# Performance work log

Measured on AMD Instinct MI355X. Metric: run time of the kernel, lower is better.

Reference implementation:

```python
import jax, jax.numpy as jnp
import numpy as np

B, S, D = 4, 2048, 1024
MULT = 4
INNER = MULT * D
E = 4          # n_expert
K = 1          # top-k
ALPHA = 0.5


def setup_inputs() -> dict:
    key = jax.random.key(0)
    ks = jax.random.split(key, 8)
    std = 0.02
    x = jax.random.normal(ks[0], (B, S, D), jnp.float32)
    W1 = jax.random.normal(ks[1], (D, INNER), jnp.float32) * std
    b1 = jnp.zeros((INNER,), jnp.float32)
    W2 = jax.random.normal(ks[2], (INNER, D), jnp.float32) * std
    b2 = jnp.zeros((D,), jnp.float32)
    Wg = jax.random.normal(ks[3], (D, E), jnp.float32) * std
    ew1 = jax.random.normal(ks[4], (E, D, INNER), jnp.float32) * std
    ew3 = jax.random.normal(ks[5], (E, D, INNER), jnp.float32) * std
    ew2 = jax.random.normal(ks[6], (E, INNER, D), jnp.float32) * std
    return {"x": x, "W1": W1, "b1": b1, "W2": W2, "b2": b2,
            "Wg": Wg, "ew1": ew1, "ew3": ew3, "ew2": ew2}


def reference(x, W1, b1, W2, b2, Wg, ew1, ew3, ew2):
    # Dense branch: Linear -> GELU (exact, torch default) -> Linear
    y_dense = jax.nn.gelu(x @ W1 + b1, approximate=False) @ W2 + b2

    # MoE branch: top-k softmax routing, SwiGLU experts
    logits = x @ Wg                                   # [B,S,E]
    probs = jax.nn.softmax(logits, axis=-1)
    topv, topi = jax.lax.top_k(probs, K)              # [B,S,K]
    gates = topv / jnp.sum(topv, axis=-1, keepdims=True)  # renormalize top-k
    onehot = jax.nn.one_hot(topi, E, dtype=x.dtype)   # [B,S,K,E]
    combine = jnp.sum(gates[..., None] * onehot, axis=-2)  # [B,S,E]

    y_moe = jnp.zeros_like(x)
    for e in range(E):  # small fixed expert count
        h = jax.nn.silu(x @ ew1[e]) * (x @ ew3[e])    # [B,S,INNER]
        y_moe = y_moe + combine[..., e:e + 1] * (h @ ew2[e])

    # Load-balancing aux loss: E * sum_e f_e * P_e
    frac = jnp.mean(jnp.sum(onehot, axis=-2), axis=(0, 1)) / K  # [E]
    pmean = jnp.mean(probs, axis=(0, 1))                        # [E]
    aux = E * jnp.sum(frac * pmean)

    y = ALPHA * y_dense + (1.0 - ALPHA) * y_moe
    return (y, aux)
```

## Files before the change

### kernel.cpp

```cpp
#include <hip/hip_runtime.h>
#include <hip/hip_bf16.h>


static constexpr int MT = 8192;
static constexpr int DD = 1024;
static constexpr int DI = 4096;

typedef float f32x4 __attribute__((ext_vector_type(4)));
typedef __bf16 bf16x8 __attribute__((ext_vector_type(8)));
typedef unsigned short u16;

__device__ __forceinline__ u16 f2bf(float f) {
    union { __hip_bfloat16 b; u16 u; } v;
    v.b = __float2bfloat16(f);
    return v.u;
}

__device__ __forceinline__ void gload_lds16(const void* g, void* l) {
    __builtin_amdgcn_global_load_lds(
        (const __attribute__((address_space(1))) void*)g,
        (__attribute__((address_space(3))) void*)l, 16, 0, 0);
}

__device__ __forceinline__ float gelu_f(float v) {
    return 0.5f * v * (1.0f + erff(v * 0.70710678118654752f));
}
__device__ __forceinline__ float silu_f(float v) {
    return v / (1.0f + expf(-v));
}

#define FENCE() asm volatile("" ::: "memory")
#define BARRIER() do { FENCE(); __builtin_amdgcn_s_barrier(); FENCE(); } while (0)
#define WAIT_LGKM0() asm volatile("s_waitcnt lgkmcnt(0)" ::: "memory")

__global__ void __launch_bounds__(256) transpose_cvt(
    const float* __restrict__ src, u16* __restrict__ dst, int K, int N,
    int pack, int packOff, size_t srcMatStride, size_t dstMatStride) {
    __shared__ u16 t[64][72];
    const float* s = src + (size_t)blockIdx.z * srcMatStride;
    u16* d = dst + (size_t)blockIdx.z * dstMatStride;
    int n0 = blockIdx.x * 64, k0 = blockIdx.y * 64;
    int tid = threadIdx.x;
    int c = tid & 15;
    int r = tid >> 4;
#pragma unroll
    for (int p = 0; p < 4; ++p) {
        int k = r + p * 16;
        float4 v = *(const float4*)(s + (size_t)(k0 + k) * N + n0 + c * 4);
        t[c * 4 + 0][k] = f2bf(v.x);
        t[c * 4 + 1][k] = f2bf(v.y);
        t[c * 4 + 2][k] = f2bf(v.z);
        t[c * 4 + 3][k] = f2bf(v.w);
    }
    __syncthreads();
    int n = tid >> 2, kc = (tid & 3) * 16;
    const uint4* p0 = (const uint4*)&t[n][kc];
    uint4 a = p0[0], b = p0[1];
    int gn = n0 + n;
    int dr = pack ? ((gn >> 5) * 64 + (gn & 31) + packOff) : gn;
    uint4* o = (uint4*)(d + (size_t)dr * K + k0 + kc);
    o[0] = a; o[1] = b;
}

__global__ void __launch_bounds__(256) gate_kernel(
    const float* __restrict__ x, const float* __restrict__ Wg,
    float* __restrict__ psum_blk, int* __restrict__ expertA) {
    int w = threadIdx.x >> 6, l = threadIdx.x & 63;
    int t = blockIdx.x * 4 + w;
    const float* xr = x + (size_t)t * DD;
    double a0 = 0, a1 = 0, a2 = 0, a3 = 0;
#pragma unroll
    for (int i = 0; i < 4; ++i) {
        int k = i * 256 + l * 4;
        float4 xv = *(const float4*)(xr + k);
        float4 w0 = *(const float4*)(Wg + (size_t)(k + 0) * 4);
        float4 w1 = *(const float4*)(Wg + (size_t)(k + 1) * 4);
        float4 w2 = *(const float4*)(Wg + (size_t)(k + 2) * 4);
        float4 w3 = *(const float4*)(Wg + (size_t)(k + 3) * 4);
        a0 += (double)xv.x * w0.x + (double)xv.y * w1.x + (double)xv.z * w2.x + (double)xv.w * w3.x;
        a1 += (double)xv.x * w0.y + (double)xv.y * w1.y + (double)xv.z * w2.y + (double)xv.w * w3.y;
        a2 += (double)xv.x * w0.z + (double)xv.y * w1.z + (double)xv.z * w2.z + (double)xv.w * w3.z;
        a3 += (double)xv.x * w0.w + (double)xv.y * w1.w + (double)xv.z * w2.w + (double)xv.w * w3.w;
    }
#pragma unroll
    for (int o = 32; o; o >>= 1) {
        a0 += __shfl_down(a0, o); a1 += __shfl_down(a1, o);
        a2 += __shfl_down(a2, o); a3 += __shfl_down(a3, o);
    }
    __shared__ float wps[4][4];
    if (l == 0) {
        double lg[4] = {a0, a1, a2, a3};
        int best = 0;
#pragma unroll
        for (int e = 1; e < 4; ++e) if (lg[e] > lg[best]) best = e;
        double m = lg[best], s = 0, p[4];
#pragma unroll
        for (int e = 0; e < 4; ++e) { p[e] = exp(lg[e] - m); s += p[e]; }
#pragma unroll
        for (int e = 0; e < 4; ++e) wps[w][e] = (float)(p[e] / s);
        expertA[t] = best;
    }
    __syncthreads();
    if (threadIdx.x < 4)
        psum_blk[blockIdx.x * 4 + threadIdx.x] =
            wps[0][threadIdx.x] + wps[1][threadIdx.x] + wps[2][threadIdx.x] + wps[3][threadIdx.x];
}

__global__ void __launch_bounds__(1024) build_lists(
    const int* __restrict__ expertA, const float* __restrict__ psum_blk,
    int* __restrict__ dstArr, int* __restrict__ rev,
    int* __restrict__ offsets, float* __restrict__ auxOut) {
    __shared__ int sc[4][1024];
    __shared__ float fs[1024];
    __shared__ float psum_s[4];
    __shared__ int tot_s[4], off_s[4];
    int tid = threadIdx.x;
    int le[8]; int c[4] = {0, 0, 0, 0};
#pragma unroll
    for (int i = 0; i < 8; ++i) { int e = expertA[tid * 8 + i]; le[i] = e; c[e]++; }
#pragma unroll
    for (int e = 0; e < 4; ++e) sc[e][tid] = c[e];
    __syncthreads();
    for (int o = 1; o < 1024; o <<= 1) {
        int v[4];
#pragma unroll
        for (int e = 0; e < 4; ++e) v[e] = (tid >= o) ? sc[e][tid - o] : 0;
        __syncthreads();
#pragma unroll
        for (int e = 0; e < 4; ++e) if (tid >= o) sc[e][tid] += v[e];
        __syncthreads();
    }
    if (tid == 0) {
        int o = 0;
#pragma unroll
        for (int e = 0; e < 4; ++e) {
            tot_s[e] = sc[e][1023]; off_s[e] = o; offsets[e] = o; o += tot_s[e];
        }
        offsets[4] = o;
    }
    __syncthreads();
    int base[4];
#pragma unroll
    for (int e = 0; e < 4; ++e) base[e] = off_s[e] + sc[e][tid] - c[e];
#pragma unroll
    for (int i = 0; i < 8; ++i) {
        int e = le[i]; int d = base[e]++; int t = tid * 8 + i;
        dstArr[t] = d; rev[d] = t;
    }
    float ps[4];
#pragma unroll
    for (int e = 0; e < 4; ++e)
        ps[e] = psum_blk[(2 * tid) * 4 + e] + psum_blk[(2 * tid + 1) * 4 + e];
    for (int e = 0; e < 4; ++e) {
        fs[tid] = ps[e]; __syncthreads();
        for (int o = 512; o; o >>= 1) { if (tid < o) fs[tid] += fs[tid + o]; __syncthreads(); }
        if (tid == 0) psum_s[e] = fs[0];
        __syncthreads();
    }
    if (tid == 0) {
        float a = 0;
#pragma unroll
        for (int e = 0; e < 4; ++e)
            a += ((float)tot_s[e] * (1.f / 8192.f)) * (psum_s[e] * (1.f / 8192.f));
        auxOut[0] = 4.f * a;
    }
}

__global__ void __launch_bounds__(256) gather_kernel(
    const float* __restrict__ x, const int* __restrict__ dstArr,
    u16* __restrict__ xb, u16* __restrict__ xg) {
    int w = threadIdx.x >> 6, l = threadIdx.x & 63;
    int t = blockIdx.x * 4 + w;
    int dst = dstArr[t];
    const float* xr = x + (size_t)t * DD;
#pragma unroll
    for (int i = 0; i < 4; ++i) {
        int k = i * 256 + l * 4;
        float4 v = *(const float4*)(xr + k);
        ushort4 u;
        u.x = f2bf(v.x); u.y = f2bf(v.y); u.z = f2bf(v.z); u.w = f2bf(v.w);
        *(ushort4*)(xb + (size_t)t * DD + k) = u;
        *(ushort4*)(xg + (size_t)dst * DD + k) = u;
    }
}

template <int MODE, int NF>
__global__ void __launch_bounds__(512, 2) gemm8(
    const u16* __restrict__ A, const u16* __restrict__ Bw,
    const float* __restrict__ bias,
    u16* __restrict__ outB, float* __restrict__ outF,
    const int* __restrict__ offsets, const int* __restrict__ rev,
    int N, int K) {
    constexpr int BN   = NF * 64;
    constexpr int WCW  = NF * 16;
    constexpr int AELT = 2 * 256 * 32;
    constexpr int BUFE = AELT + 2 * BN * 32;
    constexpr int NIB  = NF / 2;
    __shared__ u16 lds[2 * BUFE];

    const int tid = threadIdx.x;
    const int w = tid >> 6, l = tid & 63;
    const int lr = l & 15, lg = l >> 4;
    const int wr = w >> 2, wc = w & 3;

    int rowBase, rowsValid = 256;
    const u16* Bp = Bw;
    if constexpr (MODE >= 2) {
        int e = blockIdx.z;
        int off = offsets[e], cnt = offsets[e + 1] - off;
        if ((int)blockIdx.y * 256 >= cnt) return;
        rowBase = off + blockIdx.y * 256;
        rowsValid = cnt - (int)blockIdx.y * 256;
        if (rowsValid > 256) rowsValid = 256;
        Bp = Bw + (size_t)e * ((size_t)(MODE == 2 ? 2 : 1) * DD * DI);
    } else {
        rowBase = blockIdx.y * 256;
    }
    const int colBase = blockIdx.x * BN;
    const int NT = K >> 6;

    auto stageA = [&](int kt, int b, int ks) {
        const int kk = (kt << 6) + (ks << 5);
#pragma unroll
        for (int i = 0; i < 2; ++i) {
            int o = ((w << 1) + i) * 512 + (l << 3);
            int o2 = o ^ (((o >> 8) & 1) << 4);
            gload_lds16(A + (size_t)(rowBase + (o2 >> 5)) * K + kk + (o2 & 31),
                        &lds[b * BUFE + ks * 8192 + ((w << 1) + i) * 512]);
        }
    };
    auto stageB = [&](int kt, int b, int ks) {
        const int kk = (kt << 6) + (ks << 5);
#pragma unroll
        for (int i = 0; i < NIB; ++i) {
            int o = (w * NIB + i) * 512 + (l << 3);
            int o2 = o ^ (((o >> 8) & 1) << 4);
            gload_lds16(Bp + (size_t)(colBase + (o2 >> 5)) * K + kk + (o2 & 31),
                        &lds[b * BUFE + AELT + ks * (BN * 32) + (w * NIB + i) * 512]);
        }
    };

#define WAIT_VMB() do { \
    if constexpr (NF == 4) asm volatile("s_waitcnt vmcnt(4)" ::: "memory"); \
    else                   asm volatile("s_waitcnt vmcnt(3)" ::: "memory"); \
} while (0)

#define READBF(b_, ks_) do { \
    _Pragma("unroll") \
    for (int n = 0; n < NF; ++n) { \
        int e_ = (wc * WCW + n * 16 + lr) * 32 + lg * 8; \
        e_ ^= ((e_ >> 8) & 1) << 4; \
        bf[n] = *(const bf16x8*)&lds[(b_) * BUFE + AELT + (ks_) * (BN * 32) + e_]; \
    } \
} while (0)

#define READAF(b_, ks_, mq_) do { \
    _Pragma("unroll") \
    for (int m = 0; m < 4; ++m) { \
        int e_ = (wr * 128 + ((mq_) * 4 + m) * 16 + lr) * 32 + lg * 8; \
        e_ ^= ((e_ >> 8) & 1) << 4; \
        af[m] = *(const bf16x8*)&lds[(b_) * BUFE + (ks_) * 8192 + e_]; \
    } \
} while (0)

#define DOMFMA(mq_) do { \
    __builtin_amdgcn_s_setprio(1); \
    _Pragma("unroll") \
    for (int m = 0; m < 4; ++m) \
    _Pragma("unroll") \
    for (int n = 0; n < NF; ++n) \
        acc[(mq_) * 4 + m][n] = __builtin_amdgcn_mfma_f32_16x16x32_bf16( \
            bf[n], af[m], acc[(mq_) * 4 + m][n], 0, 0, 0); \
    __builtin_amdgcn_s_setprio(0); \
} while (0)

    f32x4 acc[8][NF];
#pragma unroll
    for (int m = 0; m < 8; ++m)
#pragma unroll
        for (int n = 0; n < NF; ++n) acc[m][n] = (f32x4){0.f, 0.f, 0.f, 0.f};
    bf16x8 af[4], bf[NF];

    stageA(0, 0, 0); stageB(0, 0, 0); stageA(0, 0, 1); stageB(0, 0, 1);
    stageA(1, 1, 0); stageB(1, 1, 0);
    WAIT_VMB();
    BARRIER();

    for (int t = 0; t < NT; ++t) {
        const int cb = t & 1, nb = cb ^ 1;
        const int tp1 = (t + 1 < NT) ? t + 1 : NT - 1;
        const int tp2 = (t + 2 < NT) ? t + 2 : NT - 1;
        READBF(cb, 0); READAF(cb, 0, 0); stageA(tp1, nb, 1);
        BARRIER(); WAIT_LGKM0(); DOMFMA(0); BARRIER();
        READAF(cb, 0, 1); stageB(tp1, nb, 1);
        BARRIER(); WAIT_LGKM0(); DOMFMA(1); BARRIER();
        READBF(cb, 1); READAF(cb, 1, 0); stageA(tp2, cb, 0);
        BARRIER(); WAIT_LGKM0(); DOMFMA(0); BARRIER();
        READAF(cb, 1, 1); stageB(tp2, cb, 0);
        BARRIER(); WAIT_LGKM0(); DOMFMA(1);
        WAIT_VMB();
        BARRIER();
    }

#pragma unroll
    for (int m = 0; m < 8; ++m) {
        int rloc = wr * 128 + m * 16 + lr;
        if (MODE >= 2 && rloc >= rowsValid) continue;
        size_t grow = (size_t)(rowBase + rloc);
        if constexpr (MODE == 2) {
#pragma unroll
            for (int n = 0; n < 2; ++n) {
                int col = (colBase >> 1) + wc * 32 + n * 16 + lg * 4;
                f32x4 v1 = acc[m][n], v3 = acc[m][n + 2];
                ushort4 u;
                u.x = f2bf(silu_f(v1[0]) * v3[0]);
                u.y = f2bf(silu_f(v1[1]) * v3[1]);
                u.z = f2bf(silu_f(v1[2]) * v3[2]);
                u.w = f2bf(silu_f(v1[3]) * v3[3]);
                *(ushort4*)(outB + grow * N + col) = u;
            }
        } else {
#pragma unroll
            for (int n = 0; n < NF; ++n) {
                int col = colBase + wc * WCW + n * 16 + lg * 4;
                f32x4 v = acc[m][n];
                if constexpr (MODE == 0) {
                    f32x4 bb = *(const f32x4*)(bias + col);
                    ushort4 u;
                    u.x = f2bf(gelu_f(v[0] + bb[0]));
                    u.y = f2bf(gelu_f(v[1] + bb[1]));
                    u.z = f2bf(gelu_f(v[2] + bb[2]));
                    u.w = f2bf(gelu_f(v[3] + bb[3]));
                    *(ushort4*)(outB + grow * N + col) = u;
                } else if constexpr (MODE == 1) {
                    f32x4 bb = *(const f32x4*)(bias + col);
                    f32x4 r;
#pragma unroll
                    for (int j = 0; j < 4; ++j) r[j] = 0.5f * (v[j] + bb[j]);
                    *(f32x4*)(outF + grow * N + col) = r;
                } else {
                    int tok = rev[grow];
                    f32x4* p = (f32x4*)(outF + (size_t)tok * N + col);
                    f32x4 o = *p;
#pragma unroll
                    for (int j = 0; j < 4; ++j) o[j] += 0.5f * v[j];
                    *p = o;
                }
            }
        }
    }
#undef WAIT_VMB
#undef READBF
#undef READAF
#undef DOMFMA
}

extern "C" void kernel_launch(void* const* d_in, const int* in_sizes, int n_in,
                              void* d_out, int out_size, void* d_ws, size_t ws_size,
                              hipStream_t stream) {
    const float* x   = (const float*)d_in[0];
    const float* W1  = (const float*)d_in[1];
    const float* b1  = (const float*)d_in[2];
    const float* W2  = (const float*)d_in[3];
    const float* b2  = (const float*)d_in[4];
    const float* Wg  = (const float*)d_in[5];
    const float* ew1 = (const float*)d_in[6];
    const float* ew3 = (const float*)d_in[7];
    const float* ew2 = (const float*)d_in[8];
    float* y = (float*)d_out;
    float* auxOut = y + (size_t)MT * DD;

    char* ws = (char*)d_ws;
    size_t off = 0;
    auto take = [&](size_t b) -> void* {
        void* p = ws + off;
        off += (b + 255) & ~(size_t)255;
        return p;
    };
    u16* W1t   = (u16*)take((size_t)DI * DD * 2);
    u16* W2t   = (u16*)take((size_t)DI * DD * 2);
    u16* ew13t = (u16*)take((size_t)4 * 2 * DI * DD * 2);
    u16* ew2t  = (u16*)take((size_t)4 * DI * DD * 2);
    u16* xb    = (u16*)take((size_t)MT * DD * 2);
    u16* xg    = (u16*)take((size_t)(MT + 256) * DD * 2);
    u16* hd    = (u16*)take((size_t)(MT + 256) * DI * 2);
    int* expertA  = (int*)take(MT * 4);
    int* dstArr   = (int*)take(MT * 4);
    int* revA     = (int*)take(MT * 4);
    float* psum_blk = (float*)take(2048 * 4 * 4);
    int* offsets  = (int*)take(64);
    u16* hg = hd;

    if (ws_size < off) return;

    dim3 blk(256);
    transpose_cvt<<<dim3(64, 16, 1), blk, 0, stream>>>(W1,  W1t,  DD, DI, 0, 0,  (size_t)DD * DI, (size_t)DD * DI);
    transpose_cvt<<<dim3(64, 16, 4), blk, 0, stream>>>(ew1, ew13t, DD, DI, 1, 0,  (size_t)DD * DI, (size_t)2 * DD * DI);
    transpose_cvt<<<dim3(64, 16, 4), blk, 0, stream>>>(ew3, ew13t, DD, DI, 1, 32, (size_t)DD * DI, (size_t)2 * DD * DI);
    transpose_cvt<<<dim3(16, 64, 1), blk, 0, stream>>>(W2,  W2t,  DI, DD, 0, 0,  (size_t)DD * DI, (size_t)DD * DI);
    transpose_cvt<<<dim3(16, 64, 4), blk, 0, stream>>>(ew2, ew2t, DI, DD, 0, 0,  (size_t)DD * DI, (size_t)DD * DI);
    gate_kernel<<<2048, 256, 0, stream>>>(x, Wg, psum_blk, expertA);
    build_lists<<<1, 1024, 0, stream>>>(expertA, psum_blk, dstArr, revA, offsets, auxOut);
    gather_kernel<<<2048, 256, 0, stream>>>(x, dstArr, xb, xg);
    gemm8<0, 4><<<dim3(DI / 256, MT / 256), dim3(512), 0, stream>>>(
        xb, W1t, b1, hd, nullptr, nullptr, nullptr, DI, DD);
    gemm8<1, 2><<<dim3(DD / 128, MT / 256), dim3(512), 0, stream>>>(
        hd, W2t, b2, nullptr, y, nullptr, nullptr, DD, DI);
    gemm8<2, 4><<<dim3(2 * DI / 256, MT / 256, 4), dim3(512), 0, stream>>>(
        xg, ew13t, nullptr, hg, nullptr, offsets, nullptr, DI, DD);
    gemm8<3, 2><<<dim3(DD / 128, MT / 256, 4), dim3(512), 0, stream>>>(
        hg, ew2t, nullptr, nullptr, y, offsets, revA, DD, DI);
}
```

Before: 641.1 us.

## Reuse gathered activations for dense path and use simpler down-projection GEMM

The dense first GEMM now reads the expert-sorted bf16 copy xg instead of a separate row-ordered xb, so the gather kernel writes only one bf16 copy of x. The dense hidden rows therefore come out in sorted order, and the new dense down-projection scatters them back through the reverse index. Both down-projection GEMMs (K=4096, N=1024) move from the 256x128, 512-thread double-buffered gemm8 to a new single-buffered 128x128, 256-thread kernel, which gives more blocks on the narrow output. The cost is no overlap between global loads and MFMA in the new kernel, plus scattered row writes in the dense output.

```diff
diff --git a/kernel.cpp b/kernel.cpp
--- a/kernel.cpp
+++ b/kernel.cpp
@@ -168,7 +168,7 @@
 
 __global__ void __launch_bounds__(256) gather_kernel(
     const float* __restrict__ x, const int* __restrict__ dstArr,
-    u16* __restrict__ xb, u16* __restrict__ xg) {
+    u16* __restrict__ xg) {
     int w = threadIdx.x >> 6, l = threadIdx.x & 63;
     int t = blockIdx.x * 4 + w;
     int dst = dstArr[t];
@@ -179,7 +179,6 @@
         float4 v = *(const float4*)(xr + k);
         ushort4 u;
         u.x = f2bf(v.x); u.y = f2bf(v.y); u.z = f2bf(v.z); u.w = f2bf(v.w);
-        *(ushort4*)(xb + (size_t)t * DD + k) = u;
         *(ushort4*)(xg + (size_t)dst * DD + k) = u;
     }
 }
@@ -212,7 +211,7 @@
         rowBase = off + blockIdx.y * 256;
         rowsValid = cnt - (int)blockIdx.y * 256;
         if (rowsValid > 256) rowsValid = 256;
-        Bp = Bw + (size_t)e * ((size_t)(MODE == 2 ? 2 : 1) * DD * DI);
+        Bp = Bw + (size_t)e * ((size_t)2 * DD * DI);
     } else {
         rowBase = blockIdx.y * 256;
     }
@@ -324,28 +323,13 @@
             for (int n = 0; n < NF; ++n) {
                 int col = colBase + wc * WCW + n * 16 + lg * 4;
                 f32x4 v = acc[m][n];
-                if constexpr (MODE == 0) {
-                    f32x4 bb = *(const f32x4*)(bias + col);
-                    ushort4 u;
-                    u.x = f2bf(gelu_f(v[0] + bb[0]));
-                    u.y = f2bf(gelu_f(v[1] + bb[1]));
-                    u.z = f2bf(gelu_f(v[2] + bb[2]));
-                    u.w = f2bf(gelu_f(v[3] + bb[3]));
-                    *(ushort4*)(outB + grow * N + col) = u;
-                } else if constexpr (MODE == 1) {
-                    f32x4 bb = *(const f32x4*)(bias + col);
-                    f32x4 r;
-#pragma unroll
-                    for (int j = 0; j < 4; ++j) r[j] = 0.5f * (v[j] + bb[j]);
-                    *(f32x4*)(outF + grow * N + col) = r;
-                } else {
-                    int tok = rev[grow];
-                    f32x4* p = (f32x4*)(outF + (size_t)tok * N + col);
-                    f32x4 o = *p;
-#pragma unroll
-                    for (int j = 0; j < 4; ++j) o[j] += 0.5f * v[j];
-                    *p = o;
-                }
+                f32x4 bb = *(const f32x4*)(bias + col);
+                ushort4 u;
+                u.x = f2bf(gelu_f(v[0] + bb[0]));
+                u.y = f2bf(gelu_f(v[1] + bb[1]));
+                u.z = f2bf(gelu_f(v[2] + bb[2]));
+                u.w = f2bf(gelu_f(v[3] + bb[3]));
+                *(ushort4*)(outB + grow * N + col) = u;
             }
         }
     }
@@ -353,6 +337,92 @@
 #undef READBF
 #undef READAF
 #undef DOMFMA
+}
+
+template <int DM>
+__global__ void __launch_bounds__(256) gemm97(
+    const u16* __restrict__ A, const u16* __restrict__ Bw,
+    const float* __restrict__ bias, float* __restrict__ outF,
+    const int* __restrict__ offsets, const int* __restrict__ rev,
+    int N, int K) {
+    __shared__ u16 ldsA[128 * 32];
+    __shared__ u16 ldsB[128 * 32];
+    int tid = threadIdx.x, w = tid >> 6, l = tid & 63;
+    int wr = w >> 1, wc = w & 1;
+    int rowBase, rowsValid = 128;
+    const u16* Bp = Bw;
+    if constexpr (DM == 1) {
+        int e = blockIdx.z;
+        int off = offsets[e], cnt = offsets[e + 1] - off;
+        if ((int)blockIdx.y * 128 >= cnt) return;
+        rowBase = off + blockIdx.y * 128;
+        rowsValid = cnt - (int)blockIdx.y * 128;
+        if (rowsValid > 128) rowsValid = 128;
+        Bp = Bw + (size_t)e * DD * DI;
+    } else {
+        rowBase = blockIdx.y * 128;
+    }
+    int colBase = blockIdx.x * 128;
+
+    f32x4 acc[4][4];
+#pragma unroll
+    for (int m = 0; m < 4; ++m)
+#pragma unroll
+        for (int n = 0; n < 4; ++n) acc[m][n] = (f32x4){0.f, 0.f, 0.f, 0.f};
+
+    int lr = l & 15, lg = l >> 4;
+    int ar = l >> 2, ac = (l & 3) * 8;
+
+    const int nkt = K >> 5;
+    for (int kt = 0; kt < nkt; ++kt) {
+        int k0 = kt << 5;
+        const u16* ga = A + (size_t)(rowBase + w * 32 + ar) * K + k0 + ac;
+        gload_lds16(ga, &ldsA[(w * 32) * 32]);
+        gload_lds16(ga + (size_t)16 * K, &ldsA[(w * 32 + 16) * 32]);
+        const u16* gb = Bp + (size_t)(colBase + w * 32 + ar) * K + k0 + ac;
+        gload_lds16(gb, &ldsB[(w * 32) * 32]);
+        gload_lds16(gb + (size_t)16 * K, &ldsB[(w * 32 + 16) * 32]);
+        __syncthreads();
+        bf16x8 af[4], bfr[4];
+#pragma unroll
+        for (int m = 0; m < 4; ++m)
+            af[m] = *(const bf16x8*)&ldsA[(wr * 64 + m * 16 + lr) * 32 + lg * 8];
+#pragma unroll
+        for (int n = 0; n < 4; ++n)
+            bfr[n] = *(const bf16x8*)&ldsB[(wc * 64 + n * 16 + lr) * 32 + lg * 8];
+#pragma unroll
+        for (int m = 0; m < 4; ++m)
+#pragma unroll
+            for (int n = 0; n < 4; ++n)
+                acc[m][n] = __builtin_amdgcn_mfma_f32_16x16x32_bf16(
+                    bfr[n], af[m], acc[m][n], 0, 0, 0);
+        __syncthreads();
+    }
+
+#pragma unroll
+    for (int m = 0; m < 4; ++m) {
+        int rloc = wr * 64 + m * 16 + lr;
+        if (DM == 1 && rloc >= rowsValid) continue;
+        int tok = rev[rowBase + rloc];
+#pragma unroll
+        for (int n = 0; n < 4; ++n) {
+            int col = colBase + wc * 64 + n * 16 + lg * 4;
+            f32x4 v = acc[m][n];
+            if constexpr (DM == 0) {
+                f32x4 bb = *(const f32x4*)(bias + col);
+                f32x4 r;
+#pragma unroll
+                for (int j = 0; j < 4; ++j) r[j] = 0.5f * (v[j] + bb[j]);
+                *(f32x4*)(outF + (size_t)tok * N + col) = r;
+            } else {
+                f32x4* p = (f32x4*)(outF + (size_t)tok * N + col);
+                f32x4 o = *p;
+#pragma unroll
+                for (int j = 0; j < 4; ++j) o[j] += 0.5f * v[j];
+                *p = o;
+            }
+        }
+    }
 }
 
 extern "C" void kernel_launch(void* const* d_in, const int* in_sizes, int n_in,
@@ -381,7 +451,6 @@
     u16* W2t   = (u16*)take((size_t)DI * DD * 2);
     u16* ew13t = (u16*)take((size_t)4 * 2 * DI * DD * 2);
     u16* ew2t  = (u16*)take((size_t)4 * DI * DD * 2);
-    u16* xb    = (u16*)take((size_t)MT * DD * 2);
     u16* xg    = (u16*)take((size_t)(MT + 256) * DD * 2);
     u16* hd    = (u16*)take((size_t)(MT + 256) * DI * 2);
     int* expertA  = (int*)take(MT * 4);
@@ -401,13 +470,13 @@
     transpose_cvt<<<dim3(16, 64, 4), blk, 0, stream>>>(ew2, ew2t, DI, DD, 0, 0,  (size_t)DD * DI, (size_t)DD * DI);
     gate_kernel<<<2048, 256, 0, stream>>>(x, Wg, psum_blk, expertA);
     build_lists<<<1, 1024, 0, stream>>>(expertA, psum_blk, dstArr, revA, offsets, auxOut);
-    gather_kernel<<<2048, 256, 0, stream>>>(x, dstArr, xb, xg);
+    gather_kernel<<<2048, 256, 0, stream>>>(x, dstArr, xg);
     gemm8<0, 4><<<dim3(DI / 256, MT / 256), dim3(512), 0, stream>>>(
-        xb, W1t, b1, hd, nullptr, nullptr, nullptr, DI, DD);
-    gemm8<1, 2><<<dim3(DD / 128, MT / 256), dim3(512), 0, stream>>>(
-        hd, W2t, b2, nullptr, y, nullptr, nullptr, DD, DI);
+        xg, W1t, b1, hd, nullptr, nullptr, nullptr, DI, DD);
+    gemm97<0><<<dim3(DD / 128, MT / 128), blk, 0, stream>>>(
+        hd, W2t, b2, y, nullptr, revA, DD, DI);
     gemm8<2, 4><<<dim3(2 * DI / 256, MT / 256, 4), dim3(512), 0, stream>>>(
         xg, ew13t, nullptr, hg, nullptr, offsets, nullptr, DI, DD);
-    gemm8<3, 2><<<dim3(DD / 128, MT / 256, 4), dim3(512), 0, stream>>>(
-        hg, ew2t, nullptr, nullptr, y, offsets, revA, DD, DI);
-}
+    gemm97<1><<<dim3(DD / 128, MT / 128, 4), blk, 0, stream>>>(
+        hg, ew2t, nullptr, y, offsets, revA, DD, DI);
+}
```

Measured after the change: 632.0 us. No clear change (-1.4%).
